# Optimization experiments

Measured on AMD Instinct MI355X. Metric: run time of the kernel, lower is better.

## Reference

```python
import jax, jax.numpy as jnp
import numpy as np

EPS = 1e-9


def setup_inputs() -> dict:
    key = jax.random.key(0)
    ks = jax.random.split(key, 10)
    B_N, L, S = 16, 256, 1000
    d_model, d_llm, H, d_keys = 1024, 4096, 16, 64
    dk = H * d_keys  # 1024
    return {
        "target_embedding": jax.random.normal(ks[0], (B_N, L, d_model), jnp.float32),
        "source_embedding": jax.random.normal(ks[1], (S, d_llm), jnp.float32),
        "value_embedding": jax.random.normal(ks[2], (S, d_llm), jnp.float32),
        "mask": jax.random.randint(ks[3], (B_N, L), 0, 2, jnp.int32),
        "Wq": jax.random.normal(ks[4], (dk, d_model), jnp.float32) * 0.02,
        "Wk": jax.random.normal(ks[5], (dk, d_llm), jnp.float32) * 0.02,
        "bk": jax.random.normal(ks[6], (dk,), jnp.float32) * 0.02,
        "Wv": jax.random.normal(ks[7], (dk, d_llm), jnp.float32) * 0.02,
        "bv": jax.random.normal(ks[8], (dk,), jnp.float32) * 0.02,
        "Wo": jax.random.normal(ks[9], (d_llm, dk), jnp.float32) * 0.02,
    }


def reference(target_embedding, source_embedding, value_embedding, mask,
              Wq, Wk, bk, Wv, bv, Wo):
    B_N, L, _ = target_embedding.shape
    S = source_embedding.shape[0]
    H = 16
    # projections
    q = (target_embedding @ Wq.T).reshape(B_N, L, H, -1)      # [B,L,H,E]
    k = (source_embedding @ Wk.T + bk).reshape(S, H, -1)      # [S,H,E]
    v = (value_embedding @ Wv.T + bv).reshape(S, H, -1)       # [S,H,E]
    E = q.shape[-1]
    scale = 1.0 / np.sqrt(E).astype(np.float32)
    scores = jnp.einsum('blhe,she->bhls', q, k)               # [B,H,L,S]
    A = jax.nn.softmax(scale * scores, axis=-1)               # dropout is identity in eval
    # post-softmax mask (zero out whole query rows) + renormalize
    m = mask.astype(jnp.float32)[:, None, :, None]            # [B,1,L,1]
    A = A * (1.0 - m)
    A = A / (A.sum(axis=-1, keepdims=True) + EPS)
    out = jnp.einsum('bhls,she->blhe', A, v).reshape(B_N, L, -1)
    return out @ Wo.T, A
```

## Files before the change

### kernel.cpp

```cpp
#include <hip/hip_runtime.h>

#define EPSF 1e-9f

typedef _Float16 half8 __attribute__((ext_vector_type(8)));
typedef float f32x4 __attribute__((ext_vector_type(4)));

__global__ __launch_bounds__(256) void split_planes(const float* __restrict__ in,
                                                    _Float16* __restrict__ hp,
                                                    _Float16* __restrict__ lp,
                                                    int n8) {
    int i = blockIdx.x * 256 + threadIdx.x;
    if (i >= n8) return;
    const float4* p = (const float4*)in + (size_t)i * 2;
    float4 a = p[0], b = p[1];
    float v[8] = {a.x, a.y, a.z, a.w, b.x, b.y, b.z, b.w};
    half8 hv, lv;
#pragma unroll
    for (int k = 0; k < 8; ++k) {
        _Float16 h = (_Float16)v[k];
        hv[k] = h;
        lv[k] = (_Float16)(v[k] - (float)h);
    }
    ((half8*)hp)[i] = hv;
    ((half8*)lp)[i] = lv;
}

template <bool HAS_BIAS, bool B_F32, bool OUT_PLANES>
__global__ __launch_bounds__(256, 4) void gemm_f16(
    const _Float16* __restrict__ Ahp, const _Float16* __restrict__ Alp,
    const _Float16* __restrict__ Bhp, const _Float16* __restrict__ Blp,
    const float* __restrict__ Bf,
    const float* __restrict__ bias0, const float* __restrict__ bias1,
    float* __restrict__ Cf,
    _Float16* __restrict__ Chp, _Float16* __restrict__ Clp,
    int M, int N, int K, size_t zsA, size_t zsB, size_t zsC) {
    const int z = blockIdx.z;
    Ahp += z * zsA; Alp += z * zsA;
    if (!B_F32) { Bhp += z * zsB; Blp += z * zsB; }
    else        { Bf  += z * zsB; }
    if (OUT_PLANES) { Chp += z * zsC; Clp += z * zsC; }
    const float* bias = (HAS_BIAS && z) ? bias1 : bias0;

    __shared__ __align__(16) char lds[24576];
    const int AsHo = 0, AsLo = 4096, BsHo = 8192, BsLo = 16384;

    const int tid = threadIdx.x;
    const int lane = tid & 63;
    const int w = tid >> 6;
    const int wm = w >> 1, wn = w & 1;
    const int fr = lane & 15, quad = lane >> 4;
    const int bm = blockIdx.y * 64;
    const int bn = blockIdx.x * 128;

    const int srow = tid >> 2;
    const int sslot = tid & 3;

    f32x4 acc[2][4] = {};
    half8 sAh, sAl, sBh[2], sBl[2];

#define GLOAD(k0)                                                             \
    {                                                                         \
        int gr = min(bm + srow, M - 1);                                       \
        size_t ao = (size_t)gr * K + (k0) + sslot * 8;                        \
        sAh = *(const half8*)(Ahp + ao);                                      \
        sAl = *(const half8*)(Alp + ao);                                      \
        _Pragma("unroll") for (int it = 0; it < 2; ++it) {                    \
            size_t bo = (size_t)(bn + it * 64 + srow) * K + (k0) + sslot * 8; \
            if (B_F32) {                                                      \
                float4 f0 = *(const float4*)(Bf + bo);                        \
                float4 f1 = *(const float4*)(Bf + bo + 4);                    \
                float vv[8] = {f0.x, f0.y, f0.z, f0.w, f1.x, f1.y, f1.z, f1.w}; \
                half8 hv, lv;                                                 \
                _Pragma("unroll") for (int q = 0; q < 8; ++q) {               \
                    _Float16 hh = (_Float16)vv[q];                            \
                    hv[q] = hh;                                               \
                    lv[q] = (_Float16)(vv[q] - (float)hh);                    \
                }                                                             \
                sBh[it] = hv; sBl[it] = lv;                                   \
            } else {                                                          \
                sBh[it] = *(const half8*)(Bhp + bo);                          \
                sBl[it] = *(const half8*)(Blp + bo);                          \
            }                                                                 \
        }                                                                     \
    }

    GLOAD(0);
    const int nt = K / 32;

    for (int t = 0; t < nt; ++t) {
        __syncthreads();
        *(half8*)(lds + AsHo + srow * 64 + sslot * 16) = sAh;
        *(half8*)(lds + AsLo + srow * 64 + sslot * 16) = sAl;
#pragma unroll
        for (int it = 0; it < 2; ++it) {
            int r = it * 64 + srow;
            *(half8*)(lds + BsHo + r * 64 + sslot * 16) = sBh[it];
            *(half8*)(lds + BsLo + r * 64 + sslot * 16) = sBl[it];
        }
        __syncthreads();
        if (t + 1 < nt) GLOAD((t + 1) * 32);

        half8 fah[2], fal[2], fbh[4], fbl[4];
#pragma unroll
        for (int m = 0; m < 2; ++m) {
            int off = (wm * 32 + m * 16 + fr) * 64 + quad * 16;
            fah[m] = *(const half8*)(lds + AsHo + off);
            fal[m] = *(const half8*)(lds + AsLo + off);
        }
#pragma unroll
        for (int n = 0; n < 4; ++n) {
            int off = (wn * 64 + n * 16 + fr) * 64 + quad * 16;
            fbh[n] = *(const half8*)(lds + BsHo + off);
            fbl[n] = *(const half8*)(lds + BsLo + off);
        }
#pragma unroll
        for (int m = 0; m < 2; ++m)
#pragma unroll
            for (int n = 0; n < 4; ++n) {
                acc[m][n] = __builtin_amdgcn_mfma_f32_16x16x32_f16(fal[m], fbh[n], acc[m][n], 0, 0, 0);
                acc[m][n] = __builtin_amdgcn_mfma_f32_16x16x32_f16(fah[m], fbl[n], acc[m][n], 0, 0, 0);
                acc[m][n] = __builtin_amdgcn_mfma_f32_16x16x32_f16(fah[m], fbh[n], acc[m][n], 0, 0, 0);
            }
    }
#undef GLOAD

#pragma unroll
    for (int m = 0; m < 2; ++m)
#pragma unroll
        for (int r = 0; r < 4; ++r) {
            int grow = bm + wm * 32 + m * 16 + quad * 4 + r;
            if (grow >= M) continue;
#pragma unroll
            for (int n = 0; n < 4; ++n) {
                int gcol = bn + wn * 64 + n * 16 + fr;
                float v = acc[m][n][r];
                if (HAS_BIAS) v += bias[gcol];
                if (OUT_PLANES) {
                    _Float16 hh = (_Float16)v;
                    Chp[(size_t)grow * N + gcol] = hh;
                    Clp[(size_t)grow * N + gcol] = (_Float16)(v - (float)hh);
                } else {
                    Cf[(size_t)grow * N + gcol] = v;
                }
            }
        }
}

__global__ __launch_bounds__(512) void attn_fused(
    const _Float16* __restrict__ Qh, const _Float16* __restrict__ Ql,
    const _Float16* __restrict__ Kh, const _Float16* __restrict__ Kl,
    const _Float16* __restrict__ Vh, const _Float16* __restrict__ Vl,
    const int* __restrict__ mask,
    float* __restrict__ Aout,
    _Float16* __restrict__ Owh, _Float16* __restrict__ Owl) {
    const int S = 1000, NT = 16;

    __shared__ __align__(16) char KhL[64 * 128];
    __shared__ __align__(16) char KlL[64 * 128];
    __shared__ __align__(16) _Float16 Vth[64][72];
    __shared__ __align__(16) _Float16 Vtl[64][72];
    __shared__ __align__(16) char Pb[8 * 32 * 128];

    const int tid = threadIdx.x;
    const int lane = tid & 63;
    const int w = tid >> 6;
    const int le = lane & 15;
    const int quad = lane >> 4;
    const int bh = blockIdx.x;
    const int b = bh >> 4, h = bh & 15;

#define SWZ(row, byte) ((row) * 128 + ((byte) ^ (((row) & 7) << 4)))

    half8 qh[2][2], ql[2][2];
#pragma unroll
    for (int m = 0; m < 2; ++m)
#pragma unroll
        for (int t = 0; t < 2; ++t) {
            size_t qo = ((size_t)(b * 256 + w * 32 + m * 16 + le)) * 1024 + h * 64 + t * 32 + quad * 8;
            qh[m][t] = *(const half8*)(Qh + qo);
            ql[m][t] = *(const half8*)(Ql + qo);
        }

    int mk[2][4];
#pragma unroll
    for (int m = 0; m < 2; ++m)
#pragma unroll
        for (int r = 0; r < 4; ++r)
            mk[m][r] = mask[b * 256 + w * 32 + m * 16 + quad * 4 + r];

    const int sr = tid >> 3;
    const int sc = tid & 7;
    half8 kha, kla;
    _Float16 vvh[8], vvl[8];

#define LOADK(t)                                                       \
    {                                                                  \
        int s_ = min((t) * 64 + sr, S - 1);                            \
        size_t o_ = (size_t)s_ * 1024 + h * 64 + sc * 8;               \
        kha = *(const half8*)(Kh + o_);                                \
        kla = *(const half8*)(Kl + o_);                                \
    }
#define LOADV(t)                                                       \
    {                                                                  \
        int s_ = min((t) * 64 + sr, S - 1);                            \
        size_t o_ = (size_t)s_ * 1024 + h * 64 + sc;                   \
        _Pragma("unroll") for (int i_ = 0; i_ < 8; ++i_) {             \
            vvh[i_] = Vh[o_ + 8 * i_];                                 \
            vvl[i_] = Vl[o_ + 8 * i_];                                 \
        }                                                              \
    }
#define STOREK()                                                       \
    {                                                                  \
        *(half8*)(KhL + SWZ(sr, sc * 16)) = kha;                       \
        *(half8*)(KlL + SWZ(sr, sc * 16)) = kla;                       \
    }
#define STOREV()                                                       \
    {                                                                  \
        _Pragma("unroll") for (int i_ = 0; i_ < 8; ++i_) {             \
            Vth[sc + 8 * i_][sr] = vvh[i_];                            \
            Vtl[sc + 8 * i_][sr] = vvl[i_];                            \
        }                                                              \
    }
#define SCORES(acc)                                                           \
    _Pragma("unroll") for (int j = 0; j < 4; ++j) {                           \
        int srow_ = j * 16 + le;                                              \
        half8 kh0 = *(const half8*)(KhL + SWZ(srow_, quad * 16));             \
        half8 kh1 = *(const half8*)(KhL + SWZ(srow_, 64 + quad * 16));        \
        half8 kl0 = *(const half8*)(KlL + SWZ(srow_, quad * 16));             \
        half8 kl1 = *(const half8*)(KlL + SWZ(srow_, 64 + quad * 16));        \
        _Pragma("unroll") for (int m = 0; m < 2; ++m) {                       \
            acc[m][j] = __builtin_amdgcn_mfma_f32_16x16x32_f16(ql[m][0], kh0, acc[m][j], 0, 0, 0); \
            acc[m][j] = __builtin_amdgcn_mfma_f32_16x16x32_f16(qh[m][0], kl0, acc[m][j], 0, 0, 0); \
            acc[m][j] = __builtin_amdgcn_mfma_f32_16x16x32_f16(qh[m][0], kh0, acc[m][j], 0, 0, 0); \
            acc[m][j] = __builtin_amdgcn_mfma_f32_16x16x32_f16(ql[m][1], kh1, acc[m][j], 0, 0, 0); \
            acc[m][j] = __builtin_amdgcn_mfma_f32_16x16x32_f16(qh[m][1], kl1, acc[m][j], 0, 0, 0); \
            acc[m][j] = __builtin_amdgcn_mfma_f32_16x16x32_f16(qh[m][1], kh1, acc[m][j], 0, 0, 0); \
        }                                                                     \
    }
#define SCALEACC(acc)                                                  \
    _Pragma("unroll") for (int m = 0; m < 2; ++m)                      \
        _Pragma("unroll") for (int j = 0; j < 4; ++j) acc[m][j] *= 0.125f;

    float mrun[2][4], lrun[2][4];
#pragma unroll
    for (int m = 0; m < 2; ++m)
#pragma unroll
        for (int r = 0; r < 4; ++r) { mrun[m][r] = -1e30f; lrun[m][r] = 0.f; }

    LOADK(0);
    for (int t = 0; t < NT; ++t) {
        __syncthreads();
        STOREK();
        __syncthreads();
        if (t + 1 < NT) LOADK(t + 1);

        f32x4 acc[2][4] = {};
        SCORES(acc);
        SCALEACC(acc);

        if (t == NT - 1) {
#pragma unroll
            for (int m = 0; m < 2; ++m)
#pragma unroll
                for (int j = 0; j < 4; ++j)
                    if (j * 16 + le >= 40) {
#pragma unroll
                        for (int r = 0; r < 4; ++r) acc[m][j][r] = -1e30f;
                    }
        }

        float tm[2][4];
#pragma unroll
        for (int m = 0; m < 2; ++m)
#pragma unroll
            for (int r = 0; r < 4; ++r)
                tm[m][r] = fmaxf(fmaxf(acc[m][0][r], acc[m][1][r]),
                                 fmaxf(acc[m][2][r], acc[m][3][r]));
#pragma unroll
        for (int xm = 1; xm < 16; xm <<= 1)
#pragma unroll
            for (int m = 0; m < 2; ++m)
#pragma unroll
                for (int r = 0; r < 4; ++r)
                    tm[m][r] = fmaxf(tm[m][r], __shfl_xor(tm[m][r], xm));

        float mn[2][4], ts[2][4];
#pragma unroll
        for (int m = 0; m < 2; ++m)
#pragma unroll
            for (int r = 0; r < 4; ++r) {
                mn[m][r] = fmaxf(mrun[m][r], tm[m][r]);
                float s = 0.f;
#pragma unroll
                for (int j = 0; j < 4; ++j) s += __expf(acc[m][j][r] - mn[m][r]);
                ts[m][r] = s;
            }
#pragma unroll
        for (int xm = 1; xm < 16; xm <<= 1)
#pragma unroll
            for (int m = 0; m < 2; ++m)
#pragma unroll
                for (int r = 0; r < 4; ++r)
                    ts[m][r] += __shfl_xor(ts[m][r], xm);
#pragma unroll
        for (int m = 0; m < 2; ++m)
#pragma unroll
            for (int r = 0; r < 4; ++r) {
                lrun[m][r] = lrun[m][r] * __expf(mrun[m][r] - mn[m][r]) + ts[m][r];
                mrun[m][r] = mn[m][r];
            }
    }

    float fac[2][4];
#pragma unroll
    for (int m = 0; m < 2; ++m)
#pragma unroll
        for (int r = 0; r < 4; ++r) {
            float inv = 1.0f / lrun[m][r];
            float s2 = lrun[m][r] * inv;
            fac[m][r] = mk[m][r] ? 0.0f : inv / (s2 + EPSF);
        }

    f32x4 o[2][4] = {};
    char* pb = Pb + w * 32 * 128;

    LOADK(0);
    LOADV(0);
    for (int t = 0; t < NT; ++t) {
        __syncthreads();
        STOREK();
        STOREV();
        __syncthreads();
        if (t + 1 < NT) { LOADK(t + 1); LOADV(t + 1); }

        f32x4 acc[2][4] = {};
        SCORES(acc);
        SCALEACC(acc);

        const bool last = (t == NT - 1);
#pragma unroll
        for (int m = 0; m < 2; ++m)
#pragma unroll
            for (int j = 0; j < 4; ++j) {
                bool valid = !last || (j * 16 + le < 40);
#pragma unroll
                for (int r = 0; r < 4; ++r)
                    acc[m][j][r] = valid ? __expf(acc[m][j][r] - mrun[m][r]) : 0.f;
            }

#pragma unroll
        for (int m = 0; m < 2; ++m)
#pragma unroll
            for (int r = 0; r < 4; ++r) {
                float f = fac[m][r];
                size_t ro = ((size_t)bh * 256 + w * 32 + m * 16 + quad * 4 + r) * 1000 + t * 64;
#pragma unroll
                for (int j = 0; j < 4; ++j) {
                    int sl = j * 16 + le;
                    if (!last || sl < 40) Aout[ro + sl] = acc[m][j][r] * f;
                }
            }

#pragma unroll
        for (int ks = 0; ks < 2; ++ks) {
#pragma unroll
            for (int m = 0; m < 2; ++m)
#pragma unroll
                for (int jj = 0; jj < 2; ++jj) {
                    int j = ks * 2 + jj;
#pragma unroll
                    for (int r = 0; r < 4; ++r) {
                        float e = acc[m][j][r];
                        _Float16 hh = (_Float16)e;
                        _Float16 llo = (_Float16)(e - (float)hh);
                        int q = m * 16 + quad * 4 + r;
                        int sb = (jj * 16 + le) * 2;
                        *(_Float16*)(pb + SWZ(q, sb)) = hh;
                        *(_Float16*)(pb + SWZ(q, 64 + sb)) = llo;
                    }
                }
            half8 ph[2], pl[2];
#pragma unroll
            for (int m = 0; m < 2; ++m) {
                ph[m] = *(const half8*)(pb + SWZ(m * 16 + le, quad * 16));
                pl[m] = *(const half8*)(pb + SWZ(m * 16 + le, 64 + quad * 16));
            }
#pragma unroll
            for (int n = 0; n < 4; ++n) {
                const char* vb = (const char*)Vth + (n * 16 + le) * 144 + ks * 64 + quad * 16;
                const char* vc = (const char*)Vtl + (n * 16 + le) * 144 + ks * 64 + quad * 16;
                half8 vh = *(const half8*)vb;
                half8 vl = *(const half8*)vc;
#pragma unroll
                for (int m = 0; m < 2; ++m) {
                    o[m][n] = __builtin_amdgcn_mfma_f32_16x16x32_f16(pl[m], vh, o[m][n], 0, 0, 0);
                    o[m][n] = __builtin_amdgcn_mfma_f32_16x16x32_f16(ph[m], vl, o[m][n], 0, 0, 0);
                    o[m][n] = __builtin_amdgcn_mfma_f32_16x16x32_f16(ph[m], vh, o[m][n], 0, 0, 0);
                }
            }
        }
    }

#pragma unroll
    for (int m = 0; m < 2; ++m)
#pragma unroll
        for (int r = 0; r < 4; ++r) {
            float f = fac[m][r];
            size_t ro = (size_t)(b * 256 + w * 32 + m * 16 + quad * 4 + r) * 1024 + h * 64;
#pragma unroll
            for (int n = 0; n < 4; ++n) {
                float v = o[m][n][r] * f;
                _Float16 hh = (_Float16)v;
                Owh[ro + n * 16 + le] = hh;
                Owl[ro + n * 16 + le] = (_Float16)(v - (float)hh);
            }
        }
#undef SWZ
#undef LOADK
#undef LOADV
#undef STOREK
#undef STOREV
#undef SCORES
#undef SCALEACC
}

extern "C" void kernel_launch(void* const* d_in, const int* in_sizes, int n_in,
                              void* d_out, int out_size, void* d_ws, size_t ws_size,
                              hipStream_t stream) {
    const float* target = (const float*)d_in[0];
    const float* source = (const float*)d_in[1];
    const float* value  = (const float*)d_in[2];
    const int*   mask   = (const int*)d_in[3];
    const float* Wq = (const float*)d_in[4];
    const float* Wk = (const float*)d_in[5];
    const float* bk = (const float*)d_in[6];
    const float* Wv = (const float*)d_in[7];
    const float* bv = (const float*)d_in[8];
    const float* Wo = (const float*)d_in[9];

    const int B = 16, L = 256, S = 1000, H = 16;
    const int dm = 1024, dllm = 4096, dk = 1024;
    const int BL = B * L;

    size_t need = (size_t)20873216 * sizeof(_Float16);
    if (ws_size < need) return;
    _Float16* wsf = (_Float16*)d_ws;
    _Float16* QwH = wsf;
    _Float16* QwL = QwH + 4194304;
    _Float16* KwH = QwL + 4194304;
    _Float16* VwH = KwH + 1024000;
    _Float16* KwL = VwH + 1024000;
    _Float16* VwL = KwL + 1024000;
    _Float16* OwH = VwL + 1024000;
    _Float16* OwL = OwH + 4194304;

    float* outF = (float*)d_out;
    float* Aout = outF + (size_t)BL * dllm;

    _Float16* scr = (_Float16*)Aout;
    _Float16* tgtH = scr;
    _Float16* tgtL = tgtH + 4194304;
    _Float16* srcH = tgtL + 4194304;
    _Float16* srcL = srcH + 4096000;
    _Float16* valH = srcL + 4096000;
    _Float16* valL = valH + 4096000;
    _Float16* wqH  = valL + 4096000;
    _Float16* wqL  = wqH + 1048576;
    _Float16* wkH  = wqL + 1048576;
    _Float16* wkL  = wkH + 4194304;
    _Float16* wvH  = wkL + 4194304;
    _Float16* wvL  = wvH + 4194304;

    dim3 blk(256);
#define SPLIT(src_, h_, l_, n_) \
    split_planes<<<dim3(((n_) / 8 + 255) / 256), blk, 0, stream>>>(src_, h_, l_, (n_) / 8)
    SPLIT(target, tgtH, tgtL, 4194304);
    SPLIT(source, srcH, srcL, 4096000);
    SPLIT(value,  valH, valL, 4096000);
    SPLIT(Wq,     wqH,  wqL,  1048576);
    SPLIT(Wk,     wkH,  wkL,  4194304);
    SPLIT(Wv,     wvH,  wvL,  4194304);
#undef SPLIT

    gemm_f16<false, false, true><<<dim3(dk / 128, BL / 64), blk, 0, stream>>>(
        tgtH, tgtL, wqH, wqL, nullptr, nullptr, nullptr,
        nullptr, QwH, QwL, BL, dk, dm, 0, 0, 0);

    gemm_f16<true, false, true><<<dim3(dk / 128, (S + 63) / 64, 2), blk, 0, stream>>>(
        srcH, srcL, wkH, wkL, nullptr, bk, bv,
        nullptr, KwH, KwL, S, dk, dllm,
        (size_t)8192000, (size_t)8388608, (size_t)1024000);

    attn_fused<<<dim3(B * H), dim3(512), 0, stream>>>(
        QwH, QwL, KwH, KwL, VwH, VwL, mask, Aout, OwH, OwL);

    gemm_f16<false, true, false><<<dim3(dllm / 128, BL / 64), blk, 0, stream>>>(
        OwH, OwL, nullptr, nullptr, Wo, nullptr, nullptr,
        outF, nullptr, nullptr, BL, dllm, dk, 0, 0, 0);
}
```

Before: 800.1 us.

## Double-buffer GEMMs with direct global-to-LDS loads and fuse plane-split launches

Replaces the register-staged GEMM with a double-buffered kernel that uses global_load_lds to copy tiles straight into swizzled LDS, so the next tile's load overlaps the current MFMA work. Larger 128-row tiles are used for the Q and output projections. The six split kernels become one grid-stride launch that can also pre-split Wo, so the output GEMM no longer converts fp32 to fp16 planes inline when the workspace is large enough. This needs more LDS per block, which may lower occupancy, and adds a segment lookup per element in the split kernel.

```diff
diff --git a/kernel.cpp b/kernel.cpp
--- a/kernel.cpp
+++ b/kernel.cpp
@@ -5,130 +5,139 @@
 typedef _Float16 half8 __attribute__((ext_vector_type(8)));
 typedef float f32x4 __attribute__((ext_vector_type(4)));
 
-__global__ __launch_bounds__(256) void split_planes(const float* __restrict__ in,
-                                                    _Float16* __restrict__ hp,
-                                                    _Float16* __restrict__ lp,
-                                                    int n8) {
-    int i = blockIdx.x * 256 + threadIdx.x;
-    if (i >= n8) return;
-    const float4* p = (const float4*)in + (size_t)i * 2;
-    float4 a = p[0], b = p[1];
-    float v[8] = {a.x, a.y, a.z, a.w, b.x, b.y, b.z, b.w};
-    half8 hv, lv;
-#pragma unroll
-    for (int k = 0; k < 8; ++k) {
-        _Float16 h = (_Float16)v[k];
-        hv[k] = h;
-        lv[k] = (_Float16)(v[k] - (float)h);
-    }
-    ((half8*)hp)[i] = hv;
-    ((half8*)lp)[i] = lv;
+__device__ inline void gload16(const void* gsrc, void* ldst) {
+    __builtin_amdgcn_global_load_lds(
+        (const __attribute__((address_space(1))) unsigned int*)gsrc,
+        (__attribute__((address_space(3))) unsigned int*)ldst, 16, 0, 0);
 }
 
-template <bool HAS_BIAS, bool B_F32, bool OUT_PLANES>
-__global__ __launch_bounds__(256, 4) void gemm_f16(
+struct SegPack {
+    const float* in[7];
+    _Float16* hp[7];
+    _Float16* lp[7];
+    long cum[8];
+    int nseg;
+};
+
+__global__ __launch_bounds__(256) void split_all(SegPack sp) {
+    const long total = sp.cum[sp.nseg];
+    for (long i = blockIdx.x * 256L + threadIdx.x; i < total; i += gridDim.x * 256L) {
+        int s = 0;
+        while (i >= sp.cum[s + 1]) ++s;
+        long li = i - sp.cum[s];
+        const float4* p = (const float4*)sp.in[s] + li * 2;
+        float4 a = p[0], b = p[1];
+        float v[8] = {a.x, a.y, a.z, a.w, b.x, b.y, b.z, b.w};
+        half8 hv, lv;
+#pragma unroll
+        for (int k = 0; k < 8; ++k) {
+            _Float16 h = (_Float16)v[k];
+            hv[k] = h;
+            lv[k] = (_Float16)(v[k] - (float)h);
+        }
+        ((half8*)sp.hp[s])[li] = hv;
+        ((half8*)sp.lp[s])[li] = lv;
+    }
+}
+
+template <int BM, bool HAS_BIAS, bool OUT_PLANES>
+__global__ __launch_bounds__(256) void gemm_planes(
     const _Float16* __restrict__ Ahp, const _Float16* __restrict__ Alp,
     const _Float16* __restrict__ Bhp, const _Float16* __restrict__ Blp,
-    const float* __restrict__ Bf,
     const float* __restrict__ bias0, const float* __restrict__ bias1,
-    float* __restrict__ Cf,
-    _Float16* __restrict__ Chp, _Float16* __restrict__ Clp,
-    int M, int N, int K, size_t zsA, size_t zsB, size_t zsC) {
+    float* __restrict__ Cf, _Float16* __restrict__ Chp, _Float16* __restrict__ Clp,
+    int M, int N, int K, long zsA, long zsB, long zsC) {
+    constexpr int ABY = BM * 64;
+    constexpr int BBY = 128 * 64;
+    constexpr int BUF = 2 * ABY + 2 * BBY;
+    constexpr int NC = (BUF / 1024) / 4;
+    constexpr int MF = BM / 32;
+
+    __shared__ __align__(16) char lds[2 * BUF];
+
     const int z = blockIdx.z;
-    Ahp += z * zsA; Alp += z * zsA;
-    if (!B_F32) { Bhp += z * zsB; Blp += z * zsB; }
-    else        { Bf  += z * zsB; }
-    if (OUT_PLANES) { Chp += z * zsC; Clp += z * zsC; }
+    Ahp += (long)z * zsA; Alp += (long)z * zsA;
+    Bhp += (long)z * zsB; Blp += (long)z * zsB;
+    if (OUT_PLANES) { Chp += (long)z * zsC; Clp += (long)z * zsC; }
     const float* bias = (HAS_BIAS && z) ? bias1 : bias0;
-
-    __shared__ __align__(16) char lds[24576];
-    const int AsHo = 0, AsLo = 4096, BsHo = 8192, BsLo = 16384;
 
     const int tid = threadIdx.x;
     const int lane = tid & 63;
     const int w = tid >> 6;
     const int wm = w >> 1, wn = w & 1;
     const int fr = lane & 15, quad = lane >> 4;
-    const int bm = blockIdx.y * 64;
+    const int bm = blockIdx.y * BM;
     const int bn = blockIdx.x * 128;
 
-    const int srow = tid >> 2;
-    const int sslot = tid & 3;
-
-    f32x4 acc[2][4] = {};
-    half8 sAh, sAl, sBh[2], sBl[2];
-
-#define GLOAD(k0)                                                             \
-    {                                                                         \
-        int gr = min(bm + srow, M - 1);                                       \
-        size_t ao = (size_t)gr * K + (k0) + sslot * 8;                        \
-        sAh = *(const half8*)(Ahp + ao);                                      \
-        sAl = *(const half8*)(Alp + ao);                                      \
-        _Pragma("unroll") for (int it = 0; it < 2; ++it) {                    \
-            size_t bo = (size_t)(bn + it * 64 + srow) * K + (k0) + sslot * 8; \
-            if (B_F32) {                                                      \
-                float4 f0 = *(const float4*)(Bf + bo);                        \
-                float4 f1 = *(const float4*)(Bf + bo + 4);                    \
-                float vv[8] = {f0.x, f0.y, f0.z, f0.w, f1.x, f1.y, f1.z, f1.w}; \
-                half8 hv, lv;                                                 \
-                _Pragma("unroll") for (int q = 0; q < 8; ++q) {               \
-                    _Float16 hh = (_Float16)vv[q];                            \
-                    hv[q] = hh;                                               \
-                    lv[q] = (_Float16)(vv[q] - (float)hh);                    \
-                }                                                             \
-                sBh[it] = hv; sBl[it] = lv;                                   \
-            } else {                                                          \
-                sBh[it] = *(const half8*)(Bhp + bo);                          \
-                sBl[it] = *(const half8*)(Blp + bo);                          \
-            }                                                                 \
-        }                                                                     \
-    }
-
-    GLOAD(0);
+    const _Float16* gptr[NC];
+#pragma unroll
+    for (int c = 0; c < NC; ++c) {
+        const int base = (w * NC + c) * 1024;
+        const _Float16* g;
+        int pb;
+        bool isA;
+        if (base < ABY)             { g = Ahp; pb = 0;          isA = true; }
+        else if (base < 2 * ABY)    { g = Alp; pb = ABY;        isA = true; }
+        else if (base < 2 * ABY + BBY) { g = Bhp; pb = 2 * ABY; isA = false; }
+        else                        { g = Blp; pb = 2 * ABY + BBY; isA = false; }
+        int ipb = base - pb + lane * 16;
+        int row = ipb >> 6;
+        int slot = (ipb >> 4) & 3;
+        int key = (row + (row >> 2)) & 3;
+        int grow = isA ? min(bm + row, M - 1) : (bn + row);
+        gptr[c] = g + (size_t)grow * K + (slot ^ key) * 8;
+    }
+
+#define STAGE(k0, bufb)                                                   \
+    {                                                                     \
+        _Pragma("unroll") for (int c = 0; c < NC; ++c)                    \
+            gload16(gptr[c] + (k0), (bufb) + (w * NC + c) * 1024);        \
+    }
+
+    f32x4 acc[MF][4] = {};
+
+    int cur = 0;
+    STAGE(0, lds);
+    __syncthreads();
+
     const int nt = K / 32;
-
     for (int t = 0; t < nt; ++t) {
-        __syncthreads();
-        *(half8*)(lds + AsHo + srow * 64 + sslot * 16) = sAh;
-        *(half8*)(lds + AsLo + srow * 64 + sslot * 16) = sAl;
-#pragma unroll
-        for (int it = 0; it < 2; ++it) {
-            int r = it * 64 + srow;
-            *(half8*)(lds + BsHo + r * 64 + sslot * 16) = sBh[it];
-            *(half8*)(lds + BsLo + r * 64 + sslot * 16) = sBl[it];
-        }
-        __syncthreads();
-        if (t + 1 < nt) GLOAD((t + 1) * 32);
-
-        half8 fah[2], fal[2], fbh[4], fbl[4];
-#pragma unroll
-        for (int m = 0; m < 2; ++m) {
-            int off = (wm * 32 + m * 16 + fr) * 64 + quad * 16;
-            fah[m] = *(const half8*)(lds + AsHo + off);
-            fal[m] = *(const half8*)(lds + AsLo + off);
+        char* bufb = lds + cur * BUF;
+        if (t + 1 < nt) STAGE((t + 1) * 32, lds + (cur ^ 1) * BUF);
+
+        half8 fah[MF], fal[MF], fbh[4], fbl[4];
+#pragma unroll
+        for (int m = 0; m < MF; ++m) {
+            int r = wm * (BM / 2) + m * 16 + fr;
+            int sw = (quad ^ ((r + (r >> 2)) & 3)) * 16;
+            fah[m] = *(const half8*)(bufb + r * 64 + sw);
+            fal[m] = *(const half8*)(bufb + ABY + r * 64 + sw);
         }
 #pragma unroll
         for (int n = 0; n < 4; ++n) {
-            int off = (wn * 64 + n * 16 + fr) * 64 + quad * 16;
-            fbh[n] = *(const half8*)(lds + BsHo + off);
-            fbl[n] = *(const half8*)(lds + BsLo + off);
-        }
-#pragma unroll
-        for (int m = 0; m < 2; ++m)
+            int c = wn * 64 + n * 16 + fr;
+            int sw = (quad ^ ((c + (c >> 2)) & 3)) * 16;
+            fbh[n] = *(const half8*)(bufb + 2 * ABY + c * 64 + sw);
+            fbl[n] = *(const half8*)(bufb + 2 * ABY + BBY + c * 64 + sw);
+        }
+#pragma unroll
+        for (int m = 0; m < MF; ++m)
 #pragma unroll
             for (int n = 0; n < 4; ++n) {
                 acc[m][n] = __builtin_amdgcn_mfma_f32_16x16x32_f16(fal[m], fbh[n], acc[m][n], 0, 0, 0);
                 acc[m][n] = __builtin_amdgcn_mfma_f32_16x16x32_f16(fah[m], fbl[n], acc[m][n], 0, 0, 0);
                 acc[m][n] = __builtin_amdgcn_mfma_f32_16x16x32_f16(fah[m], fbh[n], acc[m][n], 0, 0, 0);
             }
-    }
-#undef GLOAD
-
-#pragma unroll
-    for (int m = 0; m < 2; ++m)
+        __syncthreads();
+        cur ^= 1;
+    }
+#undef STAGE
+
+#pragma unroll
+    for (int m = 0; m < MF; ++m)
 #pragma unroll
         for (int r = 0; r < 4; ++r) {
-            int grow = bm + wm * 32 + m * 16 + quad * 4 + r;
+            int grow = bm + wm * (BM / 2) + m * 16 + quad * 4 + r;
             if (grow >= M) continue;
 #pragma unroll
             for (int n = 0; n < 4; ++n) {
@@ -142,6 +151,101 @@
                 } else {
                     Cf[(size_t)grow * N + gcol] = v;
                 }
+            }
+        }
+}
+
+__global__ __launch_bounds__(256, 4) void gemm_f16_bf32(
+    const _Float16* __restrict__ Ahp, const _Float16* __restrict__ Alp,
+    const float* __restrict__ Bf, float* __restrict__ Cf,
+    int M, int N, int K) {
+    __shared__ __align__(16) char lds[24576];
+    const int AsHo = 0, AsLo = 4096, BsHo = 8192, BsLo = 16384;
+
+    const int tid = threadIdx.x;
+    const int lane = tid & 63;
+    const int w = tid >> 6;
+    const int wm = w >> 1, wn = w & 1;
+    const int fr = lane & 15, quad = lane >> 4;
+    const int bm = blockIdx.y * 64;
+    const int bn = blockIdx.x * 128;
+
+    const int srow = tid >> 2;
+    const int sslot = tid & 3;
+
+    f32x4 acc[2][4] = {};
+    half8 sAh, sAl, sBh[2], sBl[2];
+
+#define GLOAD(k0)                                                              \
+    {                                                                          \
+        int gr = min(bm + srow, M - 1);                                        \
+        size_t ao = (size_t)gr * K + (k0) + sslot * 8;                         \
+        sAh = *(const half8*)(Ahp + ao);                                       \
+        sAl = *(const half8*)(Alp + ao);                                       \
+        _Pragma("unroll") for (int it = 0; it < 2; ++it) {                     \
+            size_t bo = (size_t)(bn + it * 64 + srow) * K + (k0) + sslot * 8;  \
+            float4 f0 = *(const float4*)(Bf + bo);                             \
+            float4 f1 = *(const float4*)(Bf + bo + 4);                         \
+            float vv[8] = {f0.x, f0.y, f0.z, f0.w, f1.x, f1.y, f1.z, f1.w};    \
+            half8 hv, lv;                                                      \
+            _Pragma("unroll") for (int q = 0; q < 8; ++q) {                    \
+                _Float16 hh = (_Float16)vv[q];                                 \
+                hv[q] = hh;                                                    \
+                lv[q] = (_Float16)(vv[q] - (float)hh);                         \
+            }                                                                  \
+            sBh[it] = hv; sBl[it] = lv;                                        \
+        }                                                                      \
+    }
+
+    GLOAD(0);
+    const int nt = K / 32;
+    for (int t = 0; t < nt; ++t) {
+        __syncthreads();
+        *(half8*)(lds + AsHo + srow * 64 + sslot * 16) = sAh;
+        *(half8*)(lds + AsLo + srow * 64 + sslot * 16) = sAl;
+#pragma unroll
+        for (int it = 0; it < 2; ++it) {
+            int r = it * 64 + srow;
+            *(half8*)(lds + BsHo + r * 64 + sslot * 16) = sBh[it];
+            *(half8*)(lds + BsLo + r * 64 + sslot * 16) = sBl[it];
+        }
+        __syncthreads();
+        if (t + 1 < nt) GLOAD((t + 1) * 32);
+
+        half8 fah[2], fal[2], fbh[4], fbl[4];
+#pragma unroll
+        for (int m = 0; m < 2; ++m) {
+            int off = (wm * 32 + m * 16 + fr) * 64 + quad * 16;
+            fah[m] = *(const half8*)(lds + AsHo + off);
+            fal[m] = *(const half8*)(lds + AsLo + off);
+        }
+#pragma unroll
+        for (int n = 0; n < 4; ++n) {
+            int off = (wn * 64 + n * 16 + fr) * 64 + quad * 16;
+            fbh[n] = *(const half8*)(lds + BsHo + off);
+            fbl[n] = *(const half8*)(lds + BsLo + off);
+        }
+#pragma unroll
+        for (int m = 0; m < 2; ++m)
+#pragma unroll
+            for (int n = 0; n < 4; ++n) {
+                acc[m][n] = __builtin_amdgcn_mfma_f32_16x16x32_f16(fal[m], fbh[n], acc[m][n], 0, 0, 0);
+                acc[m][n] = __builtin_amdgcn_mfma_f32_16x16x32_f16(fah[m], fbl[n], acc[m][n], 0, 0, 0);
+                acc[m][n] = __builtin_amdgcn_mfma_f32_16x16x32_f16(fah[m], fbh[n], acc[m][n], 0, 0, 0);
+            }
+    }
+#undef GLOAD
+
+#pragma unroll
+    for (int m = 0; m < 2; ++m)
+#pragma unroll
+        for (int r = 0; r < 4; ++r) {
+            int grow = bm + wm * 32 + m * 16 + quad * 4 + r;
+            if (grow >= M) continue;
+#pragma unroll
+            for (int n = 0; n < 4; ++n) {
+                int gcol = bn + wn * 64 + n * 16 + fr;
+                Cf[(size_t)grow * N + gcol] = acc[m][n][r];
             }
         }
 }
@@ -442,8 +546,11 @@
     const int dm = 1024, dllm = 4096, dk = 1024;
     const int BL = B * L;
 
-    size_t need = (size_t)20873216 * sizeof(_Float16);
-    if (ws_size < need) return;
+    const size_t need1 = (size_t)20873216 * 2;
+    const size_t need2 = (size_t)(20873216 + 8388608) * 2;
+    if (ws_size < need1) return;
+    const bool big = ws_size >= need2;
+
     _Float16* wsf = (_Float16*)d_ws;
     _Float16* QwH = wsf;
     _Float16* QwL = QwH + 4194304;
@@ -453,6 +560,8 @@
     _Float16* VwL = KwL + 1024000;
     _Float16* OwH = VwL + 1024000;
     _Float16* OwL = OwH + 4194304;
+    _Float16* WoH = OwL + 4194304;
+    _Float16* WoL = WoH + 4194304;
 
     float* outF = (float*)d_out;
     float* Aout = outF + (size_t)BL * dllm;
@@ -471,30 +580,39 @@
     _Float16* wvH  = wkL + 4194304;
     _Float16* wvL  = wvH + 4194304;
 
-    dim3 blk(256);
-#define SPLIT(src_, h_, l_, n_) \
-    split_planes<<<dim3(((n_) / 8 + 255) / 256), blk, 0, stream>>>(src_, h_, l_, (n_) / 8)
-    SPLIT(target, tgtH, tgtL, 4194304);
-    SPLIT(source, srcH, srcL, 4096000);
-    SPLIT(value,  valH, valL, 4096000);
-    SPLIT(Wq,     wqH,  wqL,  1048576);
-    SPLIT(Wk,     wkH,  wkL,  4194304);
-    SPLIT(Wv,     wvH,  wvL,  4194304);
-#undef SPLIT
-
-    gemm_f16<false, false, true><<<dim3(dk / 128, BL / 64), blk, 0, stream>>>(
-        tgtH, tgtL, wqH, wqL, nullptr, nullptr, nullptr,
+    SegPack sp;
+    const float* ins[7] = {target, source, value, Wq, Wk, Wv, Wo};
+    _Float16* hps[7] = {tgtH, srcH, valH, wqH, wkH, wvH, WoH};
+    _Float16* lps[7] = {tgtL, srcL, valL, wqL, wkL, wvL, WoL};
+    long n8s[7] = {524288, 512000, 512000, 131072, 524288, 524288, 524288};
+    sp.nseg = big ? 7 : 6;
+    sp.cum[0] = 0;
+    for (int i = 0; i < sp.nseg; ++i) {
+        sp.in[i] = ins[i]; sp.hp[i] = hps[i]; sp.lp[i] = lps[i];
+        sp.cum[i + 1] = sp.cum[i] + n8s[i];
+    }
+    for (int i = sp.nseg; i < 7; ++i) { sp.in[i] = nullptr; sp.hp[i] = nullptr; sp.lp[i] = nullptr; }
+    for (int i = sp.nseg; i < 7; ++i) sp.cum[i + 1] = sp.cum[sp.nseg];
+    split_all<<<dim3(2048), dim3(256), 0, stream>>>(sp);
+
+    gemm_planes<128, false, true><<<dim3(dk / 128, BL / 128), dim3(256), 0, stream>>>(
+        tgtH, tgtL, wqH, wqL, nullptr, nullptr,
         nullptr, QwH, QwL, BL, dk, dm, 0, 0, 0);
 
-    gemm_f16<true, false, true><<<dim3(dk / 128, (S + 63) / 64, 2), blk, 0, stream>>>(
-        srcH, srcL, wkH, wkL, nullptr, bk, bv,
+    gemm_planes<64, true, true><<<dim3(dk / 128, 16, 2), dim3(256), 0, stream>>>(
+        srcH, srcL, wkH, wkL, bk, bv,
         nullptr, KwH, KwL, S, dk, dllm,
-        (size_t)8192000, (size_t)8388608, (size_t)1024000);
+        (long)8192000, (long)8388608, (long)1024000);
 
     attn_fused<<<dim3(B * H), dim3(512), 0, stream>>>(
         QwH, QwL, KwH, KwL, VwH, VwL, mask, Aout, OwH, OwL);
 
-    gemm_f16<false, true, false><<<dim3(dllm / 128, BL / 64), blk, 0, stream>>>(
-        OwH, OwL, nullptr, nullptr, Wo, nullptr, nullptr,
-        outF, nullptr, nullptr, BL, dllm, dk, 0, 0, 0);
+    if (big) {
+        gemm_planes<128, false, false><<<dim3(dllm / 128, BL / 128), dim3(256), 0, stream>>>(
+            OwH, OwL, WoH, WoL, nullptr, nullptr,
+            outF, nullptr, nullptr, BL, dllm, dk, 0, 0, 0);
+    } else {
+        gemm_f16_bf32<<<dim3(dllm / 128, BL / 64), dim3(256), 0, stream>>>(
+            OwH, OwL, Wo, outF, BL, dllm, dk);
+    }
 }
```

Result: faster. 757.8 us (-5.3%).
